# Optimization experiments

Measured on AMD Instinct MI355X. Metric: run time of the kernel, lower is better.

The kernel has to match this reference:

```python
import jax, jax.numpy as jnp
import numpy as np

N_NODES = 20000
N_EDGES = 160000
IN_DIM = 2048
HID = 512


def setup_inputs() -> dict:
    key = jax.random.key(0)
    ks = jax.random.split(key, 12)
    s1 = 1.0 / np.sqrt(IN_DIM)
    s2 = 1.0 / np.sqrt(HID)
    return {
        "x": jax.random.normal(ks[0], (N_NODES, IN_DIM), dtype=jnp.float32),
        "edge_index": jax.random.randint(ks[1], (2, N_EDGES), 0, N_NODES, dtype=jnp.int64),
        "W1": jax.random.uniform(ks[2], (IN_DIM, HID), jnp.float32, -s1, s1),
        "b1": jax.random.uniform(ks[3], (HID,), jnp.float32, -s1, s1),
        "W2": jax.random.uniform(ks[4], (HID, HID), jnp.float32, -s2, s2),
        "b2": jax.random.uniform(ks[5], (HID,), jnp.float32, -s2, s2),
        "Wg": jax.random.uniform(ks[6], (HID, HID), jnp.float32, -s2, s2),
        "bg": jax.random.uniform(ks[7], (HID,), jnp.float32, -s2, s2),
        "Wa": jax.random.uniform(ks[8], (HID, 1), jnp.float32, -s2, s2),
        "ba": jax.random.uniform(ks[9], (1,), jnp.float32, -s2, s2),
    }


def reference(x, edge_index, W1, b1, W2, b2, Wg, bg, Wa, ba):
    # GINConv (eps=0): h = MLP((1+eps)*x + sum_{j in N(i)} x_j)
    src, dst = edge_index[0], edge_index[1]
    agg = jax.ops.segment_sum(x[src], dst, num_segments=x.shape[0])  # [N, IN_DIM]
    h = x + agg
    h = jnp.maximum(h @ W1 + b1, 0.0) @ W2 + b2  # [N, HID]
    # Gated attention pooling scores
    A = jnp.tanh(h @ Wg + bg)                    # [N, HID]
    alpha = (A @ Wa + ba)[:, 0]                  # [N]
    att_scores = jax.nn.softmax(alpha, axis=0)   # softmax over all nodes
    return (h, att_scores)
```

## Files before the change

### kernel.cpp

```cpp
#include <hip/hip_runtime.h>

typedef __attribute__((ext_vector_type(8))) __bf16 bf16x8;
typedef __attribute__((ext_vector_type(4))) __bf16 bf16x4;
typedef __attribute__((ext_vector_type(4))) float f32x4;
typedef __attribute__((ext_vector_type(8))) unsigned short u16x8;

__device__ __forceinline__ bf16x8 cvt8(float4 a, float4 b) {
    bf16x8 o;
    o[0] = (__bf16)a.x; o[1] = (__bf16)a.y; o[2] = (__bf16)a.z; o[3] = (__bf16)a.w;
    o[4] = (__bf16)b.x; o[5] = (__bf16)b.y; o[6] = (__bf16)b.z; o[7] = (__bf16)b.w;
    return o;
}
__device__ __forceinline__ bf16x4 cvt4(f32x4 v) {
    bf16x4 o;
    o[0] = (__bf16)v[0]; o[1] = (__bf16)v[1]; o[2] = (__bf16)v[2]; o[3] = (__bf16)v[3];
    return o;
}

__device__ __forceinline__ unsigned swz(int row, int s) {
    return (unsigned)((row * 64 + s * 16) ^ ((row & 8) << 2));
}

__global__ __launch_bounds__(256) void convw_pre_kernel(const float* __restrict__ W,
                                                        char* __restrict__ out, int K) {
    int t = blockIdx.x * 256 + threadIdx.x;
    if (t >= K * 512) return;
    int k = t >> 9, n = t & 511;
    int cb = n >> 8, r = n & 255, tt = k >> 5, s = (k & 31) >> 3, e = k & 7;
    size_t off = ((size_t)cb * (K >> 5) + tt) * 16384 + swz(r, s) + e * 2;
    *(__bf16*)(out + off) = (__bf16)W[t];
}

__global__ __launch_bounds__(256) void count_kernel(const int* __restrict__ dst,
                                                    int* __restrict__ counts, int E) {
    int e = blockIdx.x * 256 + threadIdx.x;
    if (e < E) atomicAdd(&counts[dst[e]], 1);
}

__global__ __launch_bounds__(1024) void scan_kernel(const int* __restrict__ counts,
                                                    int* __restrict__ offs, int N) {
    __shared__ int wsum[16], wpre[16];
    const int CH = 20;
    int tid = threadIdx.x, lane = tid & 63, wv = tid >> 6;
    int base = tid * CH;
    int s = 0;
    for (int i = 0; i < CH; i++) { int idx = base + i; s += (idx < N) ? counts[idx] : 0; }
    int run = s;
#pragma unroll
    for (int o = 1; o < 64; o <<= 1) { int v = __shfl_up(run, o, 64); if (lane >= o) run += v; }
    if (lane == 63) wsum[wv] = run;
    __syncthreads();
    if (tid == 0) { int acc = 0; for (int w = 0; w < 16; w++) { wpre[w] = acc; acc += wsum[w]; } }
    __syncthreads();
    int pre = wpre[wv] + (run - s);
    for (int i = 0; i < CH; i++) {
        int idx = base + i;
        if (idx <= N) offs[idx] = pre;
        pre += (idx < N) ? counts[idx] : 0;
    }
}

__global__ __launch_bounds__(256) void bucket_kernel(const int* __restrict__ src,
                                                     const int* __restrict__ dst,
                                                     const int* __restrict__ offs,
                                                     int* __restrict__ cursor,
                                                     int* __restrict__ eids, int E) {
    int e = blockIdx.x * 256 + threadIdx.x;
    if (e >= E) return;
    int d = dst[e];
    int pos = atomicAdd(&cursor[d], 1);
    eids[offs[d] + pos] = src[e];
}

__global__ __launch_bounds__(256) void gather_h1_kernel(const __bf16* __restrict__ y,
                                                        const int* __restrict__ offs,
                                                        const int* __restrict__ eids,
                                                        const float* __restrict__ b1,
                                                        __bf16* __restrict__ h1b) {
    const int node = blockIdx.x * 4 + (threadIdx.x >> 6);
    const int c = (threadIdx.x & 63) * 8;
    float s[8];
    bf16x8 v = *(const bf16x8*)(y + (size_t)node * 512 + c);
#pragma unroll
    for (int j = 0; j < 8; j++) s[j] = (float)v[j];
    const int beg = offs[node], end = offs[node + 1];
    for (int k = beg; k < end; k++) {
        int sn = eids[k];
        bf16x8 u = *(const bf16x8*)(y + (size_t)sn * 512 + c);
#pragma unroll
        for (int j = 0; j < 8; j++) s[j] += (float)u[j];
    }
    bf16x8 o;
#pragma unroll
    for (int j = 0; j < 8; j++) o[j] = (__bf16)fmaxf(s[j] + b1[c + j], 0.f);
    *(bf16x8*)(h1b + (size_t)node * 512 + c) = o;
}

__global__ __launch_bounds__(256) void gemm1_kernel(const float* __restrict__ X,
                                                    const char* __restrict__ Bpre,
                                                    __bf16* __restrict__ Y) {
    constexpr int KDIM = 2048, NT2 = KDIM / 64;
    __shared__ char smem[8192];
    const int tid = threadIdx.x, lane = tid & 63, wv = tid >> 6;
    const int fr = lane & 15, sec = lane >> 4, hi4 = (lane >> 4) * 4;
    const int row0 = blockIdx.x * 32;
    const char* Bp = Bpre + (size_t)blockIdx.y * 64 * 16384;

    f32x4 acc[4][2];
#pragma unroll
    for (int m = 0; m < 4; m++)
#pragma unroll
        for (int n = 0; n < 2; n++)
#pragma unroll
            for (int r = 0; r < 4; r++) acc[m][n][r] = 0.f;

    const int r_ = tid >> 3, h_ = (tid & 7) >> 2, s_ = tid & 3;
    const unsigned awz = (unsigned)(h_ * 2048) + swz(r_, s_);
    const float* Ap = X + (size_t)(row0 + r_) * KDIM + h_ * 32 + s_ * 8;

#define ASEC(b) (smem + (b) * 4096)

    {
        float4 a0 = *(const float4*)(Ap), a1 = *(const float4*)(Ap + 4);
        *(bf16x8*)(ASEC(0) + awz) = cvt8(a0, a1);
    }
    asm volatile("s_waitcnt lgkmcnt(0)" ::: "memory");
    __builtin_amdgcn_s_barrier();

    int cur = 0;
    for (int tt = 0; tt < NT2; tt++) {
        const bool more = (tt + 1 < NT2);
        float4 a0, a1;
        if (more) {
            a0 = *(const float4*)(Ap + (tt + 1) * 64);
            a1 = *(const float4*)(Ap + (tt + 1) * 64 + 4);
        }
#pragma unroll
        for (int h = 0; h < 2; h++) {
            const char* bt = Bp + (size_t)(tt * 2 + h) * 16384;
            bf16x8 wf[4], xf[2];
#pragma unroll
            for (int m = 0; m < 4; m++)
                wf[m] = *(const bf16x8*)(bt + swz(wv * 64 + m * 16 + fr, sec));
#pragma unroll
            for (int n = 0; n < 2; n++)
                xf[n] = *(const bf16x8*)(ASEC(cur) + h * 2048 + swz(n * 16 + fr, sec));
#pragma unroll
            for (int m = 0; m < 4; m++)
#pragma unroll
                for (int n = 0; n < 2; n++)
                    acc[m][n] = __builtin_amdgcn_mfma_f32_16x16x32_bf16(wf[m], xf[n], acc[m][n], 0, 0, 0);
        }
        if (more) {
            const int nxt = cur ^ 1;
            *(bf16x8*)(ASEC(nxt) + awz) = cvt8(a0, a1);
            asm volatile("s_waitcnt lgkmcnt(0)" ::: "memory");
            __builtin_amdgcn_s_barrier();
            cur = nxt;
        }
    }
#undef ASEC

#pragma unroll
    for (int n = 0; n < 2; n++) {
        int node = row0 + n * 16 + fr;
#pragma unroll
        for (int m = 0; m < 4; m++) {
            int col = blockIdx.y * 256 + wv * 64 + m * 16 + hi4;
            *(bf16x4*)(Y + (size_t)node * 512 + col) = cvt4(acc[m][n]);
        }
    }
}

__global__ __launch_bounds__(512) void mlp23_kernel(const __bf16* __restrict__ H1,
                                                    const char* __restrict__ W2p,
                                                    const float* __restrict__ b2,
                                                    const char* __restrict__ Wgp,
                                                    const float* __restrict__ bg,
                                                    const float* __restrict__ Wa,
                                                    float* __restrict__ Hout,
                                                    float* __restrict__ alpha) {
    constexpr int NT2 = 8;
    __shared__ char smem[41216];
    char* Hs = smem + 8192;
    float* aS = (float*)(smem + 40960);
    const int tid = threadIdx.x, lane = tid & 63, wv = tid >> 6;
    const int fr = lane & 15, sec = lane >> 4, hi4 = (lane >> 4) * 4;
    const long row0 = (long)blockIdx.x * 32;
    const int cbv = wv >> 2, rbase = (wv & 3) * 64;

    if (tid < 32) aS[tid] = 0.f;

    const int srow = tid >> 3, sh = (tid & 7) >> 2, ss = tid & 3;
    const unsigned awz = (unsigned)(sh * 2048) + swz(srow, ss);
    const __bf16* ApH = H1 + (row0 + srow) * 512 + sh * 32 + ss * 8;

#define ASEC(b) (smem + (b) * 4096)

    f32x4 acc[4][2];
#pragma unroll
    for (int m = 0; m < 4; m++)
#pragma unroll
        for (int n = 0; n < 2; n++)
#pragma unroll
            for (int r = 0; r < 4; r++) acc[m][n][r] = 0.f;

    if (tid < 256) {
        u16x8 v = *(const u16x8*)(ApH);
        *(u16x8*)(ASEC(0) + awz) = v;
    }
    asm volatile("s_waitcnt lgkmcnt(0)" ::: "memory");
    __builtin_amdgcn_s_barrier();

    int cur = 0;
    for (int tt = 0; tt < NT2; tt++) {
        u16x8 av;
        const bool more = (tt + 1 < NT2);
        if (more && tid < 256) av = *(const u16x8*)(ApH + (tt + 1) * 64);
#pragma unroll
        for (int h = 0; h < 2; h++) {
            const char* bt = W2p + ((size_t)cbv * 16 + tt * 2 + h) * 16384;
            bf16x8 wf[4], xf[2];
#pragma unroll
            for (int m = 0; m < 4; m++)
                wf[m] = *(const bf16x8*)(bt + swz(rbase + m * 16 + fr, sec));
#pragma unroll
            for (int n = 0; n < 2; n++)
                xf[n] = *(const bf16x8*)(ASEC(cur) + h * 2048 + swz(n * 16 + fr, sec));
#pragma unroll
            for (int m = 0; m < 4; m++)
#pragma unroll
                for (int n = 0; n < 2; n++)
                    acc[m][n] = __builtin_amdgcn_mfma_f32_16x16x32_bf16(wf[m], xf[n], acc[m][n], 0, 0, 0);
        }
        if (more) {
            const int nxt = cur ^ 1;
            if (tid < 256) *(u16x8*)(ASEC(nxt) + awz) = av;
            asm volatile("s_waitcnt lgkmcnt(0)" ::: "memory");
            __builtin_amdgcn_s_barrier();
            cur = nxt;
        }
    }

#pragma unroll
    for (int n = 0; n < 2; n++) {
        int node = n * 16 + fr;
        long gnode = row0 + node;
#pragma unroll
        for (int m = 0; m < 4; m++) {
            int hc = wv * 64 + m * 16 + hi4;
            f32x4 bv = *(const f32x4*)(b2 + hc);
            f32x4 v = acc[m][n] + bv;
            *(f32x4*)(Hout + gnode * 512 + hc) = v;
            int tt = hc >> 5, sk = (hc & 31) >> 3, e = hc & 7;
            *(bf16x4*)(Hs + tt * 2048 + swz(node, sk) + e * 2) = cvt4(v);
        }
    }
    asm volatile("s_waitcnt lgkmcnt(0)" ::: "memory");
    __builtin_amdgcn_s_barrier();

    f32x4 acc2[4][2];
#pragma unroll
    for (int m = 0; m < 4; m++)
#pragma unroll
        for (int n = 0; n < 2; n++)
#pragma unroll
            for (int r = 0; r < 4; r++) acc2[m][n][r] = 0.f;

    for (int g = 0; g < 16; g++) {
        const char* bt = Wgp + ((size_t)cbv * 16 + g) * 16384;
        bf16x8 wf[4], xf[2];
#pragma unroll
        for (int m = 0; m < 4; m++)
            wf[m] = *(const bf16x8*)(bt + swz(rbase + m * 16 + fr, sec));
#pragma unroll
        for (int n = 0; n < 2; n++)
            xf[n] = *(const bf16x8*)(Hs + g * 2048 + swz(n * 16 + fr, sec));
#pragma unroll
        for (int m = 0; m < 4; m++)
#pragma unroll
            for (int n = 0; n < 2; n++)
                acc2[m][n] = __builtin_amdgcn_mfma_f32_16x16x32_bf16(wf[m], xf[n], acc2[m][n], 0, 0, 0);
    }
#undef ASEC

#pragma unroll
    for (int n = 0; n < 2; n++) {
        float s = 0.f;
#pragma unroll
        for (int m = 0; m < 4; m++) {
            int gc = wv * 64 + m * 16 + hi4;
            f32x4 bgv = *(const f32x4*)(bg + gc);
            f32x4 wav = *(const f32x4*)(Wa + gc);
#pragma unroll
            for (int r = 0; r < 4; r++)
                s += tanhf(acc2[m][n][r] + bgv[r]) * wav[r];
        }
        s += __shfl_xor(s, 16, 64);
        s += __shfl_xor(s, 32, 64);
        if (sec == 0) atomicAdd(&aS[n * 16 + fr], s);
    }
    __syncthreads();
    if (tid < 32) alpha[row0 + tid] = aS[tid];
}

__global__ __launch_bounds__(1024) void softmax_kernel(const float* __restrict__ alpha,
                                                       float* __restrict__ att, int N) {
    __shared__ float red[16];
    __shared__ float bc[2];
    int tid = threadIdx.x, lane = tid & 63, wv = tid >> 6;
    float m = -3.4e38f;
    for (int i = tid; i < N; i += 1024) m = fmaxf(m, alpha[i]);
#pragma unroll
    for (int o = 32; o > 0; o >>= 1) m = fmaxf(m, __shfl_xor(m, o, 64));
    if (lane == 0) red[wv] = m;
    __syncthreads();
    if (tid == 0) {
        float mm = red[0];
        for (int i = 1; i < 16; i++) mm = fmaxf(mm, red[i]);
        bc[0] = mm;
    }
    __syncthreads();
    float Mx = bc[0];
    float s = 0.f;
    for (int i = tid; i < N; i += 1024) s += expf(alpha[i] - Mx);
#pragma unroll
    for (int o = 32; o > 0; o >>= 1) s += __shfl_xor(s, o, 64);
    if (lane == 0) red[wv] = s;
    __syncthreads();
    if (tid == 0) {
        float ss = 0.f;
        for (int i = 0; i < 16; i++) ss += red[i];
        bc[1] = ss;
    }
    __syncthreads();
    float inv = 1.f / bc[1];
    for (int i = tid; i < N; i += 1024) att[i] = expf(alpha[i] - Mx) * inv;
}

extern "C" void kernel_launch(void* const* d_in, const int* in_sizes, int n_in,
                              void* d_out, int out_size, void* d_ws, size_t ws_size,
                              hipStream_t stream) {
    const float* x  = (const float*)d_in[0];
    const int*   ei = (const int*)d_in[1];
    const float* W1 = (const float*)d_in[2];
    const float* b1 = (const float*)d_in[3];
    const float* W2 = (const float*)d_in[4];
    const float* b2 = (const float*)d_in[5];
    const float* Wg = (const float*)d_in[6];
    const float* bg = (const float*)d_in[7];
    const float* Wa = (const float*)d_in[8];

    const int M = 20000, IN = 2048, H = 512, E = 160000;

    char* ws = (char*)d_ws;
    __bf16* ybf   = (__bf16*)ws;
    char*  W1p    = ws + 20480000;
    char*  W2p    = ws + 22577152;
    char*  Wgp    = ws + 23101440;
    __bf16* h1b   = (__bf16*)(ws + 23625728);
    float* alpha  = (float*)(ws + 44105728);
    int*   counts = (int*)(ws + 44185728);
    int*   offs   = (int*)(ws + 44265728);
    int*   cursor = (int*)(ws + 44345732);
    int*   eids   = (int*)(ws + 44425732);

    float* hout = (float*)d_out;
    float* att  = hout + (size_t)M * H;

    convw_pre_kernel<<<4096, 256, 0, stream>>>(W1, W1p, IN);
    convw_pre_kernel<<<1024, 256, 0, stream>>>(W2, W2p, H);
    convw_pre_kernel<<<1024, 256, 0, stream>>>(Wg, Wgp, H);

    hipMemsetAsync(counts, 0, M * 4, stream);
    count_kernel<<<(E + 255) / 256, 256, 0, stream>>>(ei + E, counts, E);
    scan_kernel<<<1, 1024, 0, stream>>>(counts, offs, M);
    hipMemsetAsync(cursor, 0, M * 4, stream);
    bucket_kernel<<<(E + 255) / 256, 256, 0, stream>>>(ei, ei + E, offs, cursor, eids, E);

    gemm1_kernel<<<dim3(625, 2), 256, 0, stream>>>(x, W1p, ybf);

    gather_h1_kernel<<<5000, 256, 0, stream>>>(ybf, offs, eids, b1, h1b);

    mlp23_kernel<<<625, 512, 0, stream>>>(h1b, W2p, b2, Wgp, bg, Wa, hout, alpha);

    softmax_kernel<<<1, 1024, 0, stream>>>(alpha, att, M);
}
```

Baseline: 318.2 us.

## Use split-K with 64-row tiles in gemm1, add a partial-sum kernel

The first GEMM now uses 64-row tiles instead of 32, which doubles reuse of each weight fragment across MFMAs. The K dimension is split in two across blockIdx.z, with each half written to its own bf16 partial buffer, and a new elementwise kernel adds the two halves before the gather. The mlp23 staging store is also changed to write linearly to shared memory, moving the swizzle into the global read addressing. The trade-off is an extra bf16 round trip through memory (two partial buffers plus a sum), one more launch, and slightly more rounding error from summing two bf16 partials.

```diff
diff --git a/kernel.cpp b/kernel.cpp
--- a/kernel.cpp
+++ b/kernel.cpp
@@ -72,6 +72,18 @@
     eids[offs[d] + pos] = src[e];
 }
 
+__global__ __launch_bounds__(256) void addy_kernel(const __bf16* __restrict__ y0,
+                                                   const __bf16* __restrict__ y1,
+                                                   __bf16* __restrict__ y) {
+    size_t i = ((size_t)blockIdx.x * 256 + threadIdx.x) * 8;
+    bf16x8 a = *(const bf16x8*)(y0 + i);
+    bf16x8 b = *(const bf16x8*)(y1 + i);
+    bf16x8 o;
+#pragma unroll
+    for (int j = 0; j < 8; j++) o[j] = (__bf16)((float)a[j] + (float)b[j]);
+    *(bf16x8*)(y + i) = o;
+}
+
 __global__ __launch_bounds__(256) void gather_h1_kernel(const __bf16* __restrict__ y,
                                                         const int* __restrict__ offs,
                                                         const int* __restrict__ eids,
@@ -98,31 +110,43 @@
 
 __global__ __launch_bounds__(256) void gemm1_kernel(const float* __restrict__ X,
                                                     const char* __restrict__ Bpre,
-                                                    __bf16* __restrict__ Y) {
-    constexpr int KDIM = 2048, NT2 = KDIM / 64;
-    __shared__ char smem[8192];
+                                                    __bf16* __restrict__ Ybase, int M) {
+    constexpr int KDIM = 2048, NT2 = 16;
+    __shared__ char smem[16384];
     const int tid = threadIdx.x, lane = tid & 63, wv = tid >> 6;
     const int fr = lane & 15, sec = lane >> 4, hi4 = (lane >> 4) * 4;
-    const int row0 = blockIdx.x * 32;
-    const char* Bp = Bpre + (size_t)blockIdx.y * 64 * 16384;
-
-    f32x4 acc[4][2];
+    const long row0 = (long)blockIdx.x * 64;
+    const int kh = blockIdx.z;
+    const char* Bp = Bpre + ((size_t)blockIdx.y * 64 + (size_t)kh * 32) * 16384;
+    __bf16* Y = Ybase + (size_t)kh * 10240000;
+
+    f32x4 acc[4][4];
 #pragma unroll
     for (int m = 0; m < 4; m++)
 #pragma unroll
-        for (int n = 0; n < 2; n++)
+        for (int n = 0; n < 4; n++)
 #pragma unroll
             for (int r = 0; r < 4; r++) acc[m][n][r] = 0.f;
 
-    const int r_ = tid >> 3, h_ = (tid & 7) >> 2, s_ = tid & 3;
-    const unsigned awz = (unsigned)(h_ * 2048) + swz(r_, s_);
-    const float* Ap = X + (size_t)(row0 + r_) * KDIM + h_ * 32 + s_ * 8;
-
-#define ASEC(b) (smem + (b) * 4096)
+    const int ar_ = tid >> 2, ks = tid & 3;
+    const unsigned awz = swz(ar_, ks);
+    long arow = row0 + ar_; if (arow > (long)M - 1) arow = M - 1;
+    const float* Ap = X + arow * KDIM + kh * 1024;
+
+#define ASEC(b) (smem + (b) * 8192)
+#define LOAD_A4(d0, d1, d2, d3, t) do {                      \
+        const float* p_ = Ap + (t) * 64 + ks * 8;            \
+        d0 = *(const float4*)(p_);                           \
+        d1 = *(const float4*)(p_ + 4);                       \
+        d2 = *(const float4*)(p_ + 32);                      \
+        d3 = *(const float4*)(p_ + 36);                      \
+    } while (0)
 
     {
-        float4 a0 = *(const float4*)(Ap), a1 = *(const float4*)(Ap + 4);
+        float4 a0, a1, a2, a3;
+        LOAD_A4(a0, a1, a2, a3, 0);
         *(bf16x8*)(ASEC(0) + awz) = cvt8(a0, a1);
+        *(bf16x8*)(ASEC(0) + 4096 + awz) = cvt8(a2, a3);
     }
     asm volatile("s_waitcnt lgkmcnt(0)" ::: "memory");
     __builtin_amdgcn_s_barrier();
@@ -130,44 +154,45 @@
     int cur = 0;
     for (int tt = 0; tt < NT2; tt++) {
         const bool more = (tt + 1 < NT2);
-        float4 a0, a1;
-        if (more) {
-            a0 = *(const float4*)(Ap + (tt + 1) * 64);
-            a1 = *(const float4*)(Ap + (tt + 1) * 64 + 4);
-        }
+        float4 a0, a1, a2, a3;
+        if (more) LOAD_A4(a0, a1, a2, a3, tt + 1);
 #pragma unroll
         for (int h = 0; h < 2; h++) {
             const char* bt = Bp + (size_t)(tt * 2 + h) * 16384;
-            bf16x8 wf[4], xf[2];
+            bf16x8 wf[4], xf[4];
 #pragma unroll
             for (int m = 0; m < 4; m++)
                 wf[m] = *(const bf16x8*)(bt + swz(wv * 64 + m * 16 + fr, sec));
 #pragma unroll
-            for (int n = 0; n < 2; n++)
-                xf[n] = *(const bf16x8*)(ASEC(cur) + h * 2048 + swz(n * 16 + fr, sec));
+            for (int n = 0; n < 4; n++)
+                xf[n] = *(const bf16x8*)(ASEC(cur) + h * 4096 + swz(n * 16 + fr, sec));
 #pragma unroll
             for (int m = 0; m < 4; m++)
 #pragma unroll
-                for (int n = 0; n < 2; n++)
+                for (int n = 0; n < 4; n++)
                     acc[m][n] = __builtin_amdgcn_mfma_f32_16x16x32_bf16(wf[m], xf[n], acc[m][n], 0, 0, 0);
         }
         if (more) {
             const int nxt = cur ^ 1;
             *(bf16x8*)(ASEC(nxt) + awz) = cvt8(a0, a1);
+            *(bf16x8*)(ASEC(nxt) + 4096 + awz) = cvt8(a2, a3);
             asm volatile("s_waitcnt lgkmcnt(0)" ::: "memory");
             __builtin_amdgcn_s_barrier();
             cur = nxt;
         }
     }
 #undef ASEC
-
-#pragma unroll
-    for (int n = 0; n < 2; n++) {
-        int node = row0 + n * 16 + fr;
-#pragma unroll
-        for (int m = 0; m < 4; m++) {
-            int col = blockIdx.y * 256 + wv * 64 + m * 16 + hi4;
-            *(bf16x4*)(Y + (size_t)node * 512 + col) = cvt4(acc[m][n]);
+#undef LOAD_A4
+
+#pragma unroll
+    for (int n = 0; n < 4; n++) {
+        long node = row0 + n * 16 + fr;
+        if (node < M) {
+#pragma unroll
+            for (int m = 0; m < 4; m++) {
+                int col = blockIdx.y * 256 + wv * 64 + m * 16 + hi4;
+                *(bf16x4*)(Y + node * 512 + col) = cvt4(acc[m][n]);
+            }
         }
     }
 }
@@ -191,8 +216,12 @@
 
     if (tid < 32) aS[tid] = 0.f;
 
-    const int srow = tid >> 3, sh = (tid & 7) >> 2, ss = tid & 3;
-    const unsigned awz = (unsigned)(sh * 2048) + swz(srow, ss);
+    const int b16 = tid * 16;
+    const int sh = b16 >> 11;
+    const int bb = b16 & 2047;
+    const int srow = bb >> 6;
+    const int soff = bb & 63;
+    const int ss = (soff ^ ((srow & 8) << 2)) >> 4;
     const __bf16* ApH = H1 + (row0 + srow) * 512 + sh * 32 + ss * 8;
 
 #define ASEC(b) (smem + (b) * 4096)
@@ -207,7 +236,7 @@
 
     if (tid < 256) {
         u16x8 v = *(const u16x8*)(ApH);
-        *(u16x8*)(ASEC(0) + awz) = v;
+        *(u16x8*)(ASEC(0) + b16) = v;
     }
     asm volatile("s_waitcnt lgkmcnt(0)" ::: "memory");
     __builtin_amdgcn_s_barrier();
@@ -235,7 +264,7 @@
         }
         if (more) {
             const int nxt = cur ^ 1;
-            if (tid < 256) *(u16x8*)(ASEC(nxt) + awz) = av;
+            if (tid < 256) *(u16x8*)(ASEC(nxt) + b16) = av;
             asm volatile("s_waitcnt lgkmcnt(0)" ::: "memory");
             __builtin_amdgcn_s_barrier();
             cur = nxt;
@@ -354,16 +383,17 @@
     const int M = 20000, IN = 2048, H = 512, E = 160000;
 
     char* ws = (char*)d_ws;
-    __bf16* ybf   = (__bf16*)ws;
-    char*  W1p    = ws + 20480000;
-    char*  W2p    = ws + 22577152;
-    char*  Wgp    = ws + 23101440;
-    __bf16* h1b   = (__bf16*)(ws + 23625728);
-    float* alpha  = (float*)(ws + 44105728);
-    int*   counts = (int*)(ws + 44185728);
-    int*   offs   = (int*)(ws + 44265728);
-    int*   cursor = (int*)(ws + 44345732);
-    int*   eids   = (int*)(ws + 44425732);
+    __bf16* yp    = (__bf16*)ws;
+    __bf16* ysum  = (__bf16*)(ws + 40960000);
+    char*  W1p    = ws + 61440000;
+    char*  W2p    = ws + 63537152;
+    char*  Wgp    = ws + 64061440;
+    __bf16* h1b   = (__bf16*)(ws + 64585728);
+    float* alpha  = (float*)(ws + 85065728);
+    int*   counts = (int*)(ws + 85145728);
+    int*   offs   = (int*)(ws + 85225728);
+    int*   cursor = (int*)(ws + 85305732);
+    int*   eids   = (int*)(ws + 85385732);
 
     float* hout = (float*)d_out;
     float* att  = hout + (size_t)M * H;
@@ -378,9 +408,10 @@
     hipMemsetAsync(cursor, 0, M * 4, stream);
     bucket_kernel<<<(E + 255) / 256, 256, 0, stream>>>(ei, ei + E, offs, cursor, eids, E);
 
-    gemm1_kernel<<<dim3(625, 2), 256, 0, stream>>>(x, W1p, ybf);
-
-    gather_h1_kernel<<<5000, 256, 0, stream>>>(ybf, offs, eids, b1, h1b);
+    gemm1_kernel<<<dim3(313, 2, 2), 256, 0, stream>>>(x, W1p, yp, M);
+    addy_kernel<<<5000, 256, 0, stream>>>(yp, yp + 10240000, ysum);
+
+    gather_h1_kernel<<<5000, 256, 0, stream>>>(ysum, offs, eids, b1, h1b);
 
     mlp23_kernel<<<625, 512, 0, stream>>>(h1b, W2p, b2, Wgp, bg, Wa, hout, alpha);
 
```

New measurement: 290.1 us. 8.8% less time.
